# Kernel optimization log

Measured on AMD Instinct MI355X. Metric: run time of the kernel, lower is better.

## Reference

```python
import jax, jax.numpy as jnp
import numpy as np

NEG_SLOPE = 0.01  # torch F.leaky_relu default


def setup_inputs() -> dict:
    key = jax.random.key(0)
    k1, k2, k3, k4 = jax.random.split(key, 4)
    B, N, F_in, F_out = 16, 2048, 128, 128
    stdv = 1.0 / np.sqrt(F_out)
    h = jax.random.normal(k1, (B, N, F_in), dtype=jnp.float32)
    adj = jax.random.uniform(k2, (B, N, N), dtype=jnp.float32)
    W = jax.random.uniform(k3, (F_in, F_out), minval=-stdv, maxval=stdv, dtype=jnp.float32)
    a = jax.random.uniform(k4, (2 * F_out, 1), minval=-stdv, maxval=stdv, dtype=jnp.float32)
    return {"h": h, "adj": adj, "W": W, "a": a}


def reference(h, adj, W, a):
    # Wh: [B, N, F_out]
    Wh = jnp.matmul(h, W)
    F_out = W.shape[1]
    a1 = a[:F_out, 0]  # [F_out]
    a2 = a[F_out:, 0]  # [F_out]
    # concat-score factorizes: e[b,i,j] = leaky(Wh[b,i]@a1 + Wh[b,j]@a2)
    f1 = jnp.einsum('bnf,f->bn', Wh, a1)  # [B, N]
    f2 = jnp.einsum('bnf,f->bn', Wh, a2)  # [B, N]
    e = jax.nn.leaky_relu(f1[:, :, None] + f2[:, None, :], negative_slope=NEG_SLOPE)  # [B,N,N]
    # NOTE: original softmax is over dim=1 (row index i), faithfully preserved
    attention = jax.nn.softmax(e, axis=1)
    h_prime = jnp.einsum('bij,bjf->bif', attention, Wh)  # bmm
    return h_prime
```

## Files before the change

kernel.cpp:

```cpp
#include <hip/hip_runtime.h>

#define BB 16
#define NN 2048
#define FF 128
#define NEG 0.01f
#define CH 128
#define CL (NN / CH)

__global__ __launch_bounds__(256) void k_wh(const float* __restrict__ h,
                                            const float* __restrict__ Wg,
                                            const float* __restrict__ a,
                                            float* __restrict__ Wh,
                                            float* __restrict__ f1,
                                            float* __restrict__ f2) {
    __shared__ float Ws[64 * 128];
    __shared__ float hsT[64 * 36];

    const int tid  = threadIdx.x;
    const int fg   = tid & 31;
    const int slot = tid >> 5;
    const int f4   = fg * 4;
    const int rowBase = blockIdx.x * 32;

    float acc[4][4];
#pragma unroll
    for (int r = 0; r < 4; ++r)
#pragma unroll
        for (int c = 0; c < 4; ++c) acc[r][c] = 0.f;

    const float4* Wg4 = (const float4*)Wg;
    const float4* hg4 = (const float4*)h;

    for (int kh = 0; kh < 128; kh += 64) {
        __syncthreads();
        for (int idx = tid; idx < 64 * 32; idx += 256) {
            int kk = idx >> 5, ff = idx & 31;
            ((float4*)Ws)[kk * 32 + ff] = Wg4[(size_t)(kh + kk) * 32 + ff];
        }
#pragma unroll
        for (int pass = 0; pass < 2; ++pass) {
            int idx = pass * 256 + tid;
            int kq = idx & 15, row = idx >> 4;
            float4 h4 = hg4[(size_t)(rowBase + row) * 32 + (kh >> 2) + kq];
            hsT[(kq * 4 + 0) * 36 + row] = h4.x;
            hsT[(kq * 4 + 1) * 36 + row] = h4.y;
            hsT[(kq * 4 + 2) * 36 + row] = h4.z;
            hsT[(kq * 4 + 3) * 36 + row] = h4.w;
        }
        __syncthreads();
#pragma unroll 8
        for (int kk = 0; kk < 64; ++kk) {
            float4 wv = *(const float4*)&Ws[kk * 128 + f4];
            float4 hv = *(const float4*)&hsT[kk * 36 + slot * 4];
            acc[0][0] += hv.x * wv.x; acc[0][1] += hv.x * wv.y; acc[0][2] += hv.x * wv.z; acc[0][3] += hv.x * wv.w;
            acc[1][0] += hv.y * wv.x; acc[1][1] += hv.y * wv.y; acc[1][2] += hv.y * wv.z; acc[1][3] += hv.y * wv.w;
            acc[2][0] += hv.z * wv.x; acc[2][1] += hv.z * wv.y; acc[2][2] += hv.z * wv.z; acc[2][3] += hv.z * wv.w;
            acc[3][0] += hv.w * wv.x; acc[3][1] += hv.w * wv.y; acc[3][2] += hv.w * wv.z; acc[3][3] += hv.w * wv.w;
        }
    }

    const float4* ag4 = (const float4*)a;
    float4 a1v = ag4[fg];
    float4 a2v = ag4[32 + fg];

#pragma unroll
    for (int r = 0; r < 4; ++r) {
        int row = rowBase + slot * 4 + r;
        float4 o; o.x = acc[r][0]; o.y = acc[r][1]; o.z = acc[r][2]; o.w = acc[r][3];
        *(float4*)&Wh[(size_t)row * 128 + f4] = o;
        float p1 = acc[r][0] * a1v.x + acc[r][1] * a1v.y + acc[r][2] * a1v.z + acc[r][3] * a1v.w;
        float p2 = acc[r][0] * a2v.x + acc[r][1] * a2v.y + acc[r][2] * a2v.z + acc[r][3] * a2v.w;
#pragma unroll
        for (int m = 16; m >= 1; m >>= 1) {
            p1 += __shfl_xor(p1, m);
            p2 += __shfl_xor(p2, m);
        }
        if (fg == 0) { f1[row] = p1; f2[row] = p2; }
    }
}

__device__ __forceinline__ float wave_incl_scan(float s, int lane) {
#pragma unroll
    for (int m = 1; m <= 32; m <<= 1) {
        float o = __shfl_up(s, m);
        if (lane >= m) s += o;
    }
    return s;
}

#define WAVE_SYNC() do { __builtin_amdgcn_wave_barrier(); asm volatile("" ::: "memory"); } while (0)

__global__ __launch_bounds__(1024) void k_sort2(const float* __restrict__ f1,
                                                const float* __restrict__ f2,
                                                float* __restrict__ SF1g,
                                                float* __restrict__ PAg,
                                                float* __restrict__ SAg,
                                                float* __restrict__ SKg,
                                                int* __restrict__ PERM,
                                                int* __restrict__ KIDX,
                                                int* __restrict__ ROWS,
                                                int* __restrict__ BOFF) {
    __shared__ float sKey[NN];
    __shared__ int   sIdx[NN];
    __shared__ float wtot[16];
    __shared__ int   hist[CH];
    __shared__ int   hscan[CH + 1];
    __shared__ int   sbuf[CH];

    const int tid  = threadIdx.x;
    const int lane = tid & 63;
    const int w    = tid >> 6;
    const int b    = blockIdx.x & 15;
    const int task = blockIdx.x >> 4;

    const float* f1b = f1 + b * NN;
    const float* f2b = f2 + b * NN;

    if (task == 0) {
        for (int i = tid; i < NN; i += 1024) sKey[i] = f1b[i];
    } else {
        for (int i = tid; i < NN; i += 1024) { sKey[i] = f2b[i]; sIdx[i] = i; }
    }

    int prevj = 1024;
    for (int k = 2; k <= NN; k <<= 1) {
        for (int j = k >> 1; j > 0; j >>= 1) {
            if (j >= 128 || prevj >= 128) __syncthreads();
            else WAVE_SYNC();
            int mask = j - 1;
            int i   = ((tid & ~mask) << 1) | (tid & mask);
            int ixj = i | j;
            bool up = ((i & k) == 0);
            float av = sKey[i], bv = sKey[ixj];
            if ((av > bv) == up) {
                sKey[i] = bv; sKey[ixj] = av;
                if (task == 1) { int t2 = sIdx[i]; sIdx[i] = sIdx[ixj]; sIdx[ixj] = t2; }
            }
            prevj = j;
        }
    }
    __syncthreads();

    if (task == 0) {
        for (int i = tid; i < NN; i += 1024) SF1g[b * NN + i] = sKey[i];
        const size_t pbase = (size_t)b * (NN + 1);
        {
            float a0 = expf(NEG * sKey[2 * tid]);
            float a1 = expf(NEG * sKey[2 * tid + 1]);
            float s = a0 + a1;
            float v = wave_incl_scan(s, lane);
            if (lane == 63) wtot[w] = v;
            __syncthreads();
            float off = 0.f;
#pragma unroll
            for (int ww = 0; ww < 16; ++ww) off += (ww < w) ? wtot[ww] : 0.f;
            float excl = off + v - s;
            PAg[pbase + 2 * tid]     = excl;
            PAg[pbase + 2 * tid + 1] = excl + a0;
            if (tid == 1023) PAg[pbase + NN] = off + v;
        }
        __syncthreads();
        {
            float y0 = expf(sKey[NN - 1 - 2 * tid]);
            float y1 = expf(sKey[NN - 2 - 2 * tid]);
            float s = y0 + y1;
            float v = wave_incl_scan(s, lane);
            if (lane == 63) wtot[w] = v;
            __syncthreads();
            float off = 0.f;
#pragma unroll
            for (int ww = 0; ww < 16; ++ww) off += (ww < w) ? wtot[ww] : 0.f;
            SAg[pbase + NN - 1 - 2 * tid] = off + (v - s) + y0;
            SAg[pbase + NN - 2 - 2 * tid] = off + v;
            if (tid == 0) SAg[pbase + NN] = 0.f;
        }
    } else {
        for (int i = tid; i < NN; i += 1024) {
            SKg[b * NN + i]  = sKey[i];
            PERM[b * NN + i] = sIdx[i];
        }
        if (tid < CH) hist[tid] = 0;
        __syncthreads();
        for (int i = tid; i < NN; i += 1024) {
            float tau = -f1b[i];
            int lo = 0, hi = NN;
            while (lo < hi) { int m = (lo + hi) >> 1; if (sKey[m] <= tau) lo = m + 1; else hi = m; }
            KIDX[b * NN + i] = lo;
            int c = lo / CL;
            if (c > CH - 1) c = CH - 1;
            sIdx[i] = c;
            atomicAdd(&hist[c], 1);
        }
        __syncthreads();
        if (tid < CH) sbuf[tid] = hist[tid];
        for (int off = 1; off < CH; off <<= 1) {
            __syncthreads();
            int v = 0;
            if (tid < CH) { v = sbuf[tid]; if (tid >= off) v += sbuf[tid - off]; }
            __syncthreads();
            if (tid < CH) sbuf[tid] = v;
        }
        __syncthreads();
        if (tid == 0) hscan[0] = 0;
        if (tid < CH) hscan[tid + 1] = sbuf[tid];
        __syncthreads();
        if (tid <= CH) BOFF[b * (CH + 1) + tid] = hscan[tid];
        if (tid < CH) hist[tid] = hscan[tid];
        __syncthreads();
        for (int i = tid; i < NN; i += 1024) {
            int c = sIdx[i];
            int pos = atomicAdd(&hist[c], 1);
            ROWS[b * NN + pos] = i;
        }
    }
}

__global__ __launch_bounds__(256) void k_uw(const float* __restrict__ SF1g,
                                            const float* __restrict__ PAg,
                                            const float* __restrict__ SAg,
                                            const float* __restrict__ SKg,
                                            float* __restrict__ Uarr,
                                            float* __restrict__ Warr) {
    __shared__ float sS[NN];
    __shared__ float sP[NN + 1];
    __shared__ float sA[NN + 1];
    const int b = blockIdx.x >> 3;
    const int q = blockIdx.x & 7;
    const int tid = threadIdx.x;
    const size_t pbase = (size_t)b * (NN + 1);
    for (int i = tid; i < NN; i += 256) sS[i] = SF1g[b * NN + i];
    for (int i = tid; i < NN + 1; i += 256) { sP[i] = PAg[pbase + i]; sA[i] = SAg[pbase + i]; }
    __syncthreads();
    const int t = q * 256 + tid;
    float f2v = SKg[b * NN + t];
    float tau = -f2v;
    int lo = 0, hi = NN;
    while (lo < hi) { int m = (lo + hi) >> 1; if (sS[m] <= tau) lo = m + 1; else hi = m; }
    float eS = expf(NEG * f2v);
    float eF = expf(f2v);
    float inv = 1.0f / (eS * sP[lo] + eF * sA[lo]);
    Uarr[b * NN + t] = eF * inv;
    Warr[b * NN + t] = eS * inv;
}

__global__ __launch_bounds__(128) void k_chunk(const float* __restrict__ Wh,
                                               const float* __restrict__ Uarr,
                                               const float* __restrict__ Warr,
                                               const int* __restrict__ PERM,
                                               float* __restrict__ CU,
                                               float* __restrict__ CW) {
    int blk = blockIdx.x;
    int b = blk / CH, c = blk % CH;
    int f = threadIdx.x;
    int base = b * NN + c * CL;
    const float* Whb = Wh + (size_t)b * NN * FF;
    float aU = 0.f, aW = 0.f;
#pragma unroll
    for (int t = 0; t < CL; ++t) {
        int j = PERM[base + t];
        float uv = Uarr[base + t], wv = Warr[base + t];
        float whv = Whb[(size_t)j * FF + f];
        aU += uv * whv; aW += wv * whv;
    }
    CU[(size_t)blk * FF + f] = aU;
    CW[(size_t)blk * FF + f] = aW;
}

__global__ __launch_bounds__(128) void k_offsets(float* __restrict__ CU,
                                                 float* __restrict__ CW,
                                                 float* __restrict__ TOT) {
    int b = blockIdx.x, f = threadIdx.x;
    float aU = 0.f, aW = 0.f;
#pragma unroll 8
    for (int c = 0; c < CH; ++c) {
        size_t idx = (size_t)(b * CH + c) * FF + f;
        float tU = CU[idx], tW = CW[idx];
        CU[idx] = aU; CW[idx] = aW;
        aU += tU; aW += tW;
    }
    TOT[b * FF + f] = aU;
}

__global__ __launch_bounds__(128) void k_emit(const float* __restrict__ Wh,
                                              const float* __restrict__ Uarr,
                                              const float* __restrict__ Warr,
                                              const int* __restrict__ PERM,
                                              const float* __restrict__ CU,
                                              const float* __restrict__ CW,
                                              const float* __restrict__ TOT,
                                              const float* __restrict__ f1,
                                              const int* __restrict__ KIDX,
                                              const int* __restrict__ ROWS,
                                              const int* __restrict__ BOFF,
                                              float* __restrict__ out) {
    __shared__ float pU[CL + 1][FF];
    __shared__ float pW[CL + 1][FF];

    const int blk = blockIdx.x;
    const int b = blk / CH, c = blk % CH;
    const int f = threadIdx.x;

    float aU = CU[(size_t)blk * FF + f];
    float aW = CW[(size_t)blk * FF + f];
    const float totU = TOT[b * FF + f];

    const int base = b * NN + c * CL;
    const float* Whb = Wh + (size_t)b * NN * FF;
#pragma unroll
    for (int t = 0; t < CL; ++t) {
        pU[t][f] = aU; pW[t][f] = aW;
        int j = PERM[base + t];
        float whv = Whb[(size_t)j * FF + f];
        aU += Uarr[base + t] * whv;
        aW += Warr[base + t] * whv;
    }
    pU[CL][f] = aU; pW[CL][f] = aW;
    __syncthreads();

    const int rb = BOFF[b * (CH + 1) + c];
    const int re = BOFF[b * (CH + 1) + c + 1];
    for (int idx = rb; idx < re; ++idx) {
        int i = ROWS[b * NN + idx];
        int k = KIDX[b * NN + i];
        int r = k - c * CL;
        float f1v = f1[b * NN + i];
        float alpha = expf(NEG * f1v);
        float beta  = expf(f1v);
        out[((size_t)(b * NN + i)) * FF + f] = alpha * pW[r][f] + beta * (totU - pU[r][f]);
    }
}

extern "C" void kernel_launch(void* const* d_in, const int* in_sizes, int n_in,
                              void* d_out, int out_size, void* d_ws, size_t ws_size,
                              hipStream_t stream) {
    const float* h  = (const float*)d_in[0];
    const float* W  = (const float*)d_in[2];
    const float* a  = (const float*)d_in[3];
    float* out = (float*)d_out;

    float* ws = (float*)d_ws;
    float* Wh   = ws;  ws += (size_t)BB * NN * FF;
    float* f1   = ws;  ws += BB * NN;
    float* f2   = ws;  ws += BB * NN;
    float* SF1  = ws;  ws += BB * NN;
    float* PA   = ws;  ws += BB * (NN + 1);
    float* SA   = ws;  ws += BB * (NN + 1);
    float* SK   = ws;  ws += BB * NN;
    float* Uarr = ws;  ws += BB * NN;
    float* Warr = ws;  ws += BB * NN;
    float* CU   = ws;  ws += (size_t)BB * CH * FF;
    float* CW   = ws;  ws += (size_t)BB * CH * FF;
    float* TOT  = ws;  ws += BB * FF;
    int* PERM = (int*)ws;  ws += BB * NN;
    int* KIDX = (int*)ws;  ws += BB * NN;
    int* ROWS = (int*)ws;  ws += BB * NN;
    int* BOFF = (int*)ws;

    k_wh     <<<(BB * NN) / 32, 256, 0, stream>>>(h, W, a, Wh, f1, f2);
    k_sort2  <<<2 * BB, 1024, 0, stream>>>(f1, f2, SF1, PA, SA, SK, PERM, KIDX, ROWS, BOFF);
    k_uw     <<<BB * 8, 256, 0, stream>>>(SF1, PA, SA, SK, Uarr, Warr);
    k_chunk  <<<BB * CH, 128, 0, stream>>>(Wh, Uarr, Warr, PERM, CU, CW);
    k_offsets<<<BB, 128, 0, stream>>>(CU, CW, TOT);
    k_emit   <<<BB * CH, 128, 0, stream>>>(Wh, Uarr, Warr, PERM, CU, CW, TOT, f1, KIDX, ROWS, BOFF, out);
}
```

Baseline: 386.3 us.

## Fuse chunk, offset and emit kernels into one cooperative kernel with grid sync

Replaces the three last launches (chunk partial sums, offset scan, emit) with one cooperative kernel that uses grid-wide syncs. Each block keeps its per-step prefix sums in shared memory, so the emit phase no longer re-gathers Wh rows to rebuild them. The change removes two launch boundaries and a second gather pass. In exchange it adds two grid barriers, a serial scan that only one block per batch performs while the rest wait, and more shared memory per block; if the cooperative launch fails it falls back to the old three kernels.

```diff
diff --git a/kernel.cpp b/kernel.cpp
--- a/kernel.cpp
+++ b/kernel.cpp
@@ -1,4 +1,7 @@
 #include <hip/hip_runtime.h>
+#include <hip/hip_cooperative_groups.h>
+
+namespace cg = cooperative_groups;
 
 #define BB 16
 #define NN 2048
@@ -243,6 +246,73 @@
     Warr[b * NN + t] = eS * inv;
 }
 
+__global__ __launch_bounds__(128, 4) void k_fused(const float* __restrict__ Wh,
+                                                  const float* __restrict__ Uarr,
+                                                  const float* __restrict__ Warr,
+                                                  const int* __restrict__ PERM,
+                                                  float* __restrict__ CU,
+                                                  float* __restrict__ CW,
+                                                  float* __restrict__ TOT,
+                                                  const float* __restrict__ f1,
+                                                  const int* __restrict__ KIDX,
+                                                  const int* __restrict__ ROWS,
+                                                  const int* __restrict__ BOFF,
+                                                  float* __restrict__ out) {
+    __shared__ float pU[CL + 1][FF];
+    __shared__ float pW[CL + 1][FF];
+
+    const int blk = blockIdx.x;
+    const int b = blk / CH, c = blk % CH;
+    const int f = threadIdx.x;
+
+    const int base = b * NN + c * CL;
+    const float* Whb = Wh + (size_t)b * NN * FF;
+    float aU = 0.f, aW = 0.f;
+#pragma unroll
+    for (int t = 0; t < CL; ++t) {
+        pU[t][f] = aU; pW[t][f] = aW;
+        int j = PERM[base + t];
+        float whv = Whb[(size_t)j * FF + f];
+        aU += Uarr[base + t] * whv;
+        aW += Warr[base + t] * whv;
+    }
+    pU[CL][f] = aU; pW[CL][f] = aW;
+    CU[(size_t)blk * FF + f] = aU;
+    CW[(size_t)blk * FF + f] = aW;
+
+    cg::this_grid().sync();
+
+    if (c == 0) {
+        float sU = 0.f, sW = 0.f;
+#pragma unroll 8
+        for (int cc = 0; cc < CH; ++cc) {
+            size_t idx = (size_t)(b * CH + cc) * FF + f;
+            float tU = CU[idx], tW = CW[idx];
+            CU[idx] = sU; CW[idx] = sW;
+            sU += tU; sW += tW;
+        }
+        TOT[b * FF + f] = sU;
+    }
+
+    cg::this_grid().sync();
+
+    const float offU = CU[(size_t)blk * FF + f];
+    const float offW = CW[(size_t)blk * FF + f];
+    const float totU = TOT[b * FF + f];
+    const int rb = BOFF[b * (CH + 1) + c];
+    const int re = BOFF[b * (CH + 1) + c + 1];
+    for (int idx = rb; idx < re; ++idx) {
+        int i = ROWS[b * NN + idx];
+        int k = KIDX[b * NN + i];
+        int r = k - c * CL;
+        float f1v = f1[b * NN + i];
+        float alpha = expf(NEG * f1v);
+        float beta  = expf(f1v);
+        out[((size_t)(b * NN + i)) * FF + f] =
+            alpha * (offW + pW[r][f]) + beta * (totU - (offU + pU[r][f]));
+    }
+}
+
 __global__ __launch_bounds__(128) void k_chunk(const float* __restrict__ Wh,
                                                const float* __restrict__ Uarr,
                                                const float* __restrict__ Warr,
@@ -356,10 +426,25 @@
     int* ROWS = (int*)ws;  ws += BB * NN;
     int* BOFF = (int*)ws;
 
-    k_wh     <<<(BB * NN) / 32, 256, 0, stream>>>(h, W, a, Wh, f1, f2);
-    k_sort2  <<<2 * BB, 1024, 0, stream>>>(f1, f2, SF1, PA, SA, SK, PERM, KIDX, ROWS, BOFF);
-    k_uw     <<<BB * 8, 256, 0, stream>>>(SF1, PA, SA, SK, Uarr, Warr);
-    k_chunk  <<<BB * CH, 128, 0, stream>>>(Wh, Uarr, Warr, PERM, CU, CW);
-    k_offsets<<<BB, 128, 0, stream>>>(CU, CW, TOT);
-    k_emit   <<<BB * CH, 128, 0, stream>>>(Wh, Uarr, Warr, PERM, CU, CW, TOT, f1, KIDX, ROWS, BOFF, out);
-}
+    k_wh    <<<(BB * NN) / 32, 256, 0, stream>>>(h, W, a, Wh, f1, f2);
+    k_sort2 <<<2 * BB, 1024, 0, stream>>>(f1, f2, SF1, PA, SA, SK, PERM, KIDX, ROWS, BOFF);
+    k_uw    <<<BB * 8, 256, 0, stream>>>(SF1, PA, SA, SK, Uarr, Warr);
+
+    {
+        const float* WhC = Wh; const float* UaC = Uarr; const float* WaC = Warr;
+        const int* PeC = PERM; const float* f1C = f1; const int* KiC = KIDX;
+        const int* RoC = ROWS; const int* BoC = BOFF;
+        void* args[] = {(void*)&WhC, (void*)&UaC, (void*)&WaC, (void*)&PeC,
+                        (void*)&CU, (void*)&CW, (void*)&TOT, (void*)&f1C,
+                        (void*)&KiC, (void*)&RoC, (void*)&BoC, (void*)&out};
+        hipError_t cerr = hipLaunchCooperativeKernel(
+            reinterpret_cast<const void*>(&k_fused),
+            dim3(BB * CH), dim3(128), args, 0, stream);
+        if (cerr != hipSuccess) {
+            k_chunk  <<<BB * CH, 128, 0, stream>>>(Wh, Uarr, Warr, PERM, CU, CW);
+            k_offsets<<<BB, 128, 0, stream>>>(CU, CW, TOT);
+            k_emit   <<<BB * CH, 128, 0, stream>>>(Wh, Uarr, Warr, PERM, CU, CW, TOT,
+                                                   f1, KIDX, ROWS, BOFF, out);
+        }
+    }
+}
```

Result: slower. 726.6 us (+88.1%).
